# Kernel optimization log

Measured on AMD Instinct MI355X. Metric: run time of the kernel, lower is better.

Reference implementation:

```python
import jax, jax.numpy as jnp
import numpy as np

B, T, I, H, K = 32, 1024, 512, 512, 2


def _causal_conv1d(x_bit, w_hik, b_h):
    # x_bit: [B, I, T]; left-pad K-1 zeros (ConstantPad1d((K-1, 0)))
    xp = jnp.pad(x_bit, ((0, 0), (0, 0), (K - 1, 0)))
    y = jax.lax.conv_general_dilated(
        xp, w_hik, window_strides=(1,), padding='VALID',
        dimension_numbers=('NCH', 'OIH', 'NCH'))  # [B, H, T]
    return y + b_h[None, :, None]


def setup_inputs() -> dict:
    key = jax.random.key(0)
    k1, k2, k3 = jax.random.split(key, 3)
    bound = 1.0 / np.sqrt(I * K)  # torch Conv1d default init scale
    return {
        'inputs': jax.random.normal(k1, (B, T, I), dtype=jnp.float32),
        'init_state': jnp.zeros((B, H), dtype=jnp.float32),
        'Wz': jax.random.uniform(k2, (H, I, K), jnp.float32, -bound, bound),
        'bz': jnp.zeros((H,), dtype=jnp.float32),
        'Wf': jax.random.uniform(k3, (H, I, K), jnp.float32, -bound, bound),
        'bf': jnp.zeros((H,), dtype=jnp.float32),
    }


def reference(inputs, init_state, Wz, bz, Wf, bf):
    # init_state is accepted but unused in the original forward (mode='f').
    x = inputs.transpose(0, 2, 1)                      # [B, I, T]
    raw_f = _causal_conv1d(x, Wf, bf).transpose(0, 2, 1)  # [B, T, H]
    raw_z = _causal_conv1d(x, Wz, bz).transpose(0, 2, 1)  # [B, T, H]

    log_f = jax.nn.log_sigmoid(raw_f)
    log_one_minus_f = jax.nn.log_sigmoid(-raw_f)
    log_z = jax.nn.log_sigmoid(raw_z)

    # recurrent_gates[t] = sum_{s>t} log_f[s]  (suffix sum of log_f over time, excluding t=0 shift)
    rg = log_f[:, 1:, :]                               # [B, T-1, H]
    cs = jnp.cumsum(rg, axis=1)
    rg = rg - cs + cs[:, -1:, :]
    rg = jnp.concatenate([rg, jnp.zeros((inputs.shape[0], 1, rg.shape[2]), dtype=rg.dtype)], axis=1)  # [B, T, H]

    log_hidden = jax.lax.cumlogsumexp(log_z + log_one_minus_f + rg, axis=1)
    hidden = jnp.exp(log_hidden - rg)
    return hidden
```

## Files before the change

### kernel.cpp

```cpp
#include <hip/hip_runtime.h>
#include <hip/hip_bf16.h>
#include <cstddef>
#include <cstdint>

#define B_  32
#define T_  1024
#define I_  512
#define H_  512
#define M_  (B_ * T_)
#define TP_ 1025

typedef __bf16 bf16x8  __attribute__((ext_vector_type(8)));
typedef float  floatx4 __attribute__((ext_vector_type(4)));
typedef unsigned short ushort8v __attribute__((ext_vector_type(8)));
typedef unsigned long long u64;

__device__ __forceinline__ unsigned short f2bf(float f) {
    uint32_t u = __float_as_uint(f);
    return (unsigned short)((u + 0x7FFFu + ((u >> 16) & 1u)) >> 16);
}
__device__ __forceinline__ float sigm(float x) {
    return __builtin_amdgcn_rcpf(1.f + __expf(-x));
}

#define GLL(src, dst) __builtin_amdgcn_global_load_lds( \
    (const __attribute__((address_space(1))) void*)(src), \
    (__attribute__((address_space(3))) void*)(dst), 16, 0, 0)

#define NB_BUILD 8200
#define NB_PACK  512
#define NB_ZERO  256

__global__ __launch_bounds__(256) void prep(const float* __restrict__ x,
                                            const float* __restrict__ Wf,
                                            const float* __restrict__ Wz,
                                            unsigned short* __restrict__ Ab2,
                                            unsigned short* __restrict__ Wq,
                                            uint4* __restrict__ HpubZ,
                                            uint32_t* __restrict__ cnt) {
    if (blockIdx.x < NB_BUILD) {
        int g = blockIdx.x * 256 + threadIdx.x;
        int idx8 = g << 3;
        int row = idx8 >> 9;
        int col = idx8 & 511;
        int b    = (int)((unsigned)row / TP_);
        int trow = row - b * TP_;
        ushort8v o = {0, 0, 0, 0, 0, 0, 0, 0};
        if (trow > 0) {
            const float* src = &x[((size_t)b * T_ + (trow - 1)) * I_ + col];
            float4 v0 = *(const float4*)src;
            float4 v1 = *(const float4*)(src + 4);
            o[0] = f2bf(v0.x); o[1] = f2bf(v0.y); o[2] = f2bf(v0.z); o[3] = f2bf(v0.w);
            o[4] = f2bf(v1.x); o[5] = f2bf(v1.y); o[6] = f2bf(v1.z); o[7] = f2bf(v1.w);
        }
        *(ushort8v*)&Ab2[(size_t)idx8] = o;
    } else if (blockIdx.x < NB_BUILD + NB_PACK) {
        int cid = (blockIdx.x - NB_BUILD) * 256 + threadIdx.x;
        int lane = cid & 63;
        int c    = (cid >> 6) & 3;
        int wn   = (cid >> 8) & 1;
        int ksub = (cid >> 9) & 31;
        int ni   = (cid >> 14) & 3;
        int gate = (cid >> 16) & 1;
        int n_col = ni * 128 + wn * 64 + c * 16 + (lane & 15);
        const float* G = gate ? Wz : Wf;
        ushort8v o;
        #pragma unroll
        for (int j = 0; j < 8; ++j) {
            int k   = ksub * 32 + (lane >> 4) * 8 + j;
            int tap = k >> 9;
            int i   = k & 511;
            o[j] = f2bf(G[n_col * (I_ * 2) + i * 2 + tap]);
        }
        *(ushort8v*)&Wq[(size_t)cid * 8] = o;
    } else {
        int g = (blockIdx.x - NB_BUILD - NB_PACK) * 256 + threadIdx.x;
        HpubZ[g] = make_uint4(0, 0, 0, 0);
        if (g == 0) *cnt = 0;
    }
}

__global__ __launch_bounds__(256, 2) void mfma_gemm_scan(
        const unsigned short* __restrict__ Ab2,
        const unsigned short* __restrict__ Wq,
        const float* __restrict__ biasF,
        const float* __restrict__ biasZ,
        float* __restrict__ out,
        u64* __restrict__ Hpub,
        uint32_t* __restrict__ counter) {
    __shared__ unsigned short smem[24576];
    __shared__ uint32_t vid_s;

    const int tid = threadIdx.x;
    if (tid == 0) vid_s = atomicAdd(counter, 1u);
    __syncthreads();
    const int vid   = (int)vid_s;
    const int low3  = vid & 7;
    const int ni    = (vid >> 3) & 3;
    const int rem   = vid >> 5;
    const int pos   = rem >> 2;
    const int b     = ((rem & 3) << 3) | low3;
    const int chain = ni * 32 + b;
    const int h0    = ni * 128;
    const int browBase = b * TP_ + pos * 128;

    const int lane = tid & 63;
    const int wave = tid >> 6;
    const int wm   = wave >> 1, wn = wave & 1;
    const int lm   = lane & 15, quad = lane >> 4;

    const int c0 = wave * 128 + lane;
    const int c1 = c0 + 64;
    const int r0 = c0 >> 2, q0 = (c0 & 3) ^ ((r0 >> 2) & 3);
    const int r1 = c1 >> 2, q1 = (c1 & 3) ^ ((r1 >> 2) & 3);

    const unsigned short* pA0 = Ab2 + (size_t)(browBase + r0) * 512 + q0 * 8;
    const unsigned short* pA1 = Ab2 + (size_t)(browBase + r1) * 512 + q1 * 8;

    unsigned short* dA0 = smem + wave * 1024;
    unsigned short* dA1 = smem + wave * 1024 + 512;

    const unsigned short* wq = Wq + ni * 131072 + wn * 2048 + lane * 8;

    int offA[4];
    #pragma unroll
    for (int r = 0; r < 4; ++r) {
        int ml = wm * 64 + r * 16 + lm;
        offA[r] = (4 * ml + (quad ^ ((ml >> 2) & 3))) * 8;
    }

    floatx4 accF[4][4] = {};
    floatx4 accZ[4][4] = {};

    for (int kt2 = 0; kt2 < 16; ++kt2) {
        const int tap = kt2 >> 3;
        const int i0  = (kt2 & 7) * 64;
        #pragma unroll
        for (int s = 0; s < 2; ++s) {
            const int aoff = tap * 512 + i0 + s * 32;
            GLL(pA0 + aoff, dA0 + s * 4096);
            GLL(pA1 + aoff, dA1 + s * 4096);
        }
        __syncthreads();

        #pragma unroll
        for (int s = 0; s < 2; ++s) {
            const int ksub = kt2 * 2 + s;
            const unsigned short* wqk = wq + ksub * 4096;
            bf16x8 af[4], bF[4], bZ[4];
            #pragma unroll
            for (int c = 0; c < 4; ++c) {
                bF[c] = *(const bf16x8*)(wqk + c * 512);
                bZ[c] = *(const bf16x8*)(wqk + 524288 + c * 512);
            }
            #pragma unroll
            for (int r = 0; r < 4; ++r) af[r] = *(const bf16x8*)(smem + s * 4096 + offA[r]);
            #pragma unroll
            for (int r = 0; r < 4; ++r) {
                #pragma unroll
                for (int c = 0; c < 4; ++c) {
                    accF[r][c] = __builtin_amdgcn_mfma_f32_16x16x32_bf16(
                                    af[r], bF[c], accF[r][c], 0, 0, 0);
                    accZ[r][c] = __builtin_amdgcn_mfma_f32_16x16x32_bf16(
                                    af[r], bZ[c], accZ[r][c], 0, 0, 0);
                }
            }
        }
        __syncthreads();
    }

    float bfv[4], bzv[4];
    #pragma unroll
    for (int c = 0; c < 4; ++c) {
        int hc = h0 + wn * 64 + c * 16 + lm;
        bfv[c] = biasF[hc];
        bzv[c] = biasZ[hc];
    }

    float2* seg  = (float2*)smem;
    float*  hinL = (float*)&smem[16384];

    #pragma unroll
    for (int r = 0; r < 4; ++r) {
        const int sid = wm * 16 + r * 4 + quad;
        #pragma unroll
        for (int c = 0; c < 4; ++c) {
            float A = 1.f, C = 0.f;
            #pragma unroll
            for (int v = 0; v < 4; ++v) {
                float f = sigm(accF[r][c][v] + bfv[c]);
                float z = sigm(accZ[r][c][v] + bzv[c]);
                accF[r][c][v] = f;
                accZ[r][c][v] = z;
                A *= f;
                C = fmaf(f, C - z, z);
            }
            seg[sid * 128 + wn * 64 + c * 16 + lm] = make_float2(A, C);
        }
    }
    __syncthreads();

    float Hin = 0.f;
    if (tid < 128) {
        float At = 1.f, Ct = 0.f;
        #pragma unroll 8
        for (int s = 0; s < 32; ++s) {
            float2 sc = seg[s * 128 + tid];
            Ct = fmaf(sc.x, Ct, sc.y);
            At *= sc.x;
        }
        if (pos > 0) {
            u64* p = &Hpub[((size_t)(pos - 1) * 128 + chain) * 128 + tid];
            u64 v;
            while (((v = atomicAdd(p, 0ull)) >> 32) == 0ull)
                __builtin_amdgcn_s_sleep(2);
            Hin = __uint_as_float((uint32_t)v);
        }
        if (pos < 7) {
            float Hout = fmaf(At, Hin, Ct);
            u64 pv = 0x100000000ull | (u64)__float_as_uint(Hout);
            atomicExch(&Hpub[((size_t)pos * 128 + chain) * 128 + tid], pv);
        }
        float run = Hin;
        #pragma unroll 8
        for (int s = 0; s < 32; ++s) {
            hinL[s * 128 + tid] = run;
            float2 sc = seg[s * 128 + tid];
            run = fmaf(sc.x, run, sc.y);
        }
    }
    __syncthreads();

    const int rowBase = b * T_ + pos * 128;
    #pragma unroll
    for (int r = 0; r < 4; ++r) {
        const int sid = wm * 16 + r * 4 + quad;
        #pragma unroll
        for (int c = 0; c < 4; ++c) {
            const int hc = h0 + wn * 64 + c * 16 + lm;
            float hs = hinL[sid * 128 + (hc - h0)];
            #pragma unroll
            for (int v = 0; v < 4; ++v) {
                float f = accF[r][c][v];
                float z = accZ[r][c][v];
                hs = fmaf(f, hs - z, z);
                const size_t row = (size_t)(rowBase + wm * 64 + r * 16 + quad * 4 + v);
                out[row * H_ + hc] = hs;
            }
        }
    }
}

extern "C" void kernel_launch(void* const* d_in, const int* in_sizes, int n_in,
                              void* d_out, int out_size, void* d_ws, size_t ws_size,
                              hipStream_t stream) {
    const float* x  = (const float*)d_in[0];
    const float* Wz = (const float*)d_in[2];
    const float* bz = (const float*)d_in[3];
    const float* Wf = (const float*)d_in[4];
    const float* bf = (const float*)d_in[5];
    float* out = (float*)d_out;

    char* ws = (char*)d_ws;
    unsigned short* Ab2  = (unsigned short*)(ws);
    unsigned short* Wq   = (unsigned short*)(ws + (size_t)34 * 1024 * 1024);
    u64*            Hpub = (u64*)(ws + (size_t)36 * 1024 * 1024);
    uint32_t*       cnt  = (uint32_t*)(ws + (size_t)37 * 1024 * 1024);

    prep<<<NB_BUILD + NB_PACK + NB_ZERO, 256, 0, stream>>>(
        x, Wf, Wz, Ab2, Wq, (uint4*)Hpub, cnt);

    mfma_gemm_scan<<<1024, 256, 0, stream>>>(Ab2, Wq, bf, bz, out, Hpub, cnt);
}
```

Baseline: 202.1 us.

## Load A fragments directly from global with register double-buffering, drop LDS staging

Replaces the LDS staging of the A tile (global_load_lds plus two barriers per k-step) with direct per-lane global loads of A fragments into registers. Both A and B fragments are double-buffered in registers so the next k-substep's loads are issued before the current MFMAs. This removes the per-iteration __syncthreads and LDS traffic, at the cost of more VGPRs and redundant global A loads across the two wn waves, which now rely on cache.

```diff
diff --git a/kernel.cpp b/kernel.cpp
--- a/kernel.cpp
+++ b/kernel.cpp
@@ -22,10 +22,6 @@
 __device__ __forceinline__ float sigm(float x) {
     return __builtin_amdgcn_rcpf(1.f + __expf(-x));
 }
-
-#define GLL(src, dst) __builtin_amdgcn_global_load_lds( \
-    (const __attribute__((address_space(1))) void*)(src), \
-    (__attribute__((address_space(3))) void*)(dst), 16, 0, 0)
 
 #define NB_BUILD 8200
 #define NB_PACK  512
@@ -109,64 +105,53 @@
     const int wm   = wave >> 1, wn = wave & 1;
     const int lm   = lane & 15, quad = lane >> 4;
 
-    const int c0 = wave * 128 + lane;
-    const int c1 = c0 + 64;
-    const int r0 = c0 >> 2, q0 = (c0 & 3) ^ ((r0 >> 2) & 3);
-    const int r1 = c1 >> 2, q1 = (c1 & 3) ^ ((r1 >> 2) & 3);
-
-    const unsigned short* pA0 = Ab2 + (size_t)(browBase + r0) * 512 + q0 * 8;
-    const unsigned short* pA1 = Ab2 + (size_t)(browBase + r1) * 512 + q1 * 8;
-
-    unsigned short* dA0 = smem + wave * 1024;
-    unsigned short* dA1 = smem + wave * 1024 + 512;
-
-    const unsigned short* wq = Wq + ni * 131072 + wn * 2048 + lane * 8;
-
-    int offA[4];
-    #pragma unroll
-    for (int r = 0; r < 4; ++r) {
-        int ml = wm * 64 + r * 16 + lm;
-        offA[r] = (4 * ml + (quad ^ ((ml >> 2) & 3))) * 8;
-    }
+    const unsigned short* pA[4];
+    #pragma unroll
+    for (int r = 0; r < 4; ++r)
+        pA[r] = Ab2 + (size_t)(browBase + wm * 64 + r * 16 + lm) * 512 + quad * 8;
+
+    const unsigned short* bqF = Wq + ni * 131072 + wn * 2048 + lane * 8;
+    const unsigned short* bqZ = bqF + 524288;
+
+    bf16x8 af[2][4], bF[2][4], bZ[2][4];
+
+#define LOADS(KSUB, BUF) do {                                            \
+        const int _ao = (((KSUB) >> 4) * 512) + (((KSUB) & 15) * 32);    \
+        _Pragma("unroll")                                                \
+        for (int _r = 0; _r < 4; ++_r)                                   \
+            af[BUF][_r] = *(const bf16x8*)(pA[_r] + _ao);                \
+        const unsigned short* _pF = bqF + (KSUB) * 4096;                 \
+        const unsigned short* _pZ = bqZ + (KSUB) * 4096;                 \
+        _Pragma("unroll")                                                \
+        for (int _c = 0; _c < 4; ++_c) {                                 \
+            bF[BUF][_c] = *(const bf16x8*)(_pF + _c * 512);              \
+            bZ[BUF][_c] = *(const bf16x8*)(_pZ + _c * 512);              \
+        }                                                                \
+    } while (0)
+
+#define MFMAS(BUF) do {                                                  \
+        _Pragma("unroll")                                                \
+        for (int _r = 0; _r < 4; ++_r) {                                 \
+            _Pragma("unroll")                                            \
+            for (int _c = 0; _c < 4; ++_c) {                             \
+                accF[_r][_c] = __builtin_amdgcn_mfma_f32_16x16x32_bf16(  \
+                    af[BUF][_r], bF[BUF][_c], accF[_r][_c], 0, 0, 0);    \
+                accZ[_r][_c] = __builtin_amdgcn_mfma_f32_16x16x32_bf16(  \
+                    af[BUF][_r], bZ[BUF][_c], accZ[_r][_c], 0, 0, 0);    \
+            }                                                            \
+        }                                                                \
+    } while (0)
 
     floatx4 accF[4][4] = {};
     floatx4 accZ[4][4] = {};
 
-    for (int kt2 = 0; kt2 < 16; ++kt2) {
-        const int tap = kt2 >> 3;
-        const int i0  = (kt2 & 7) * 64;
-        #pragma unroll
-        for (int s = 0; s < 2; ++s) {
-            const int aoff = tap * 512 + i0 + s * 32;
-            GLL(pA0 + aoff, dA0 + s * 4096);
-            GLL(pA1 + aoff, dA1 + s * 4096);
-        }
-        __syncthreads();
-
-        #pragma unroll
-        for (int s = 0; s < 2; ++s) {
-            const int ksub = kt2 * 2 + s;
-            const unsigned short* wqk = wq + ksub * 4096;
-            bf16x8 af[4], bF[4], bZ[4];
-            #pragma unroll
-            for (int c = 0; c < 4; ++c) {
-                bF[c] = *(const bf16x8*)(wqk + c * 512);
-                bZ[c] = *(const bf16x8*)(wqk + 524288 + c * 512);
-            }
-            #pragma unroll
-            for (int r = 0; r < 4; ++r) af[r] = *(const bf16x8*)(smem + s * 4096 + offA[r]);
-            #pragma unroll
-            for (int r = 0; r < 4; ++r) {
-                #pragma unroll
-                for (int c = 0; c < 4; ++c) {
-                    accF[r][c] = __builtin_amdgcn_mfma_f32_16x16x32_bf16(
-                                    af[r], bF[c], accF[r][c], 0, 0, 0);
-                    accZ[r][c] = __builtin_amdgcn_mfma_f32_16x16x32_bf16(
-                                    af[r], bZ[c], accZ[r][c], 0, 0, 0);
-                }
-            }
-        }
-        __syncthreads();
+    LOADS(0, 0);
+    for (int kk2 = 0; kk2 < 16; ++kk2) {
+        const int ksub = kk2 * 2;
+        LOADS(ksub + 1, 1);
+        MFMAS(0);
+        if (kk2 < 15) LOADS(ksub + 2, 0);
+        MFMAS(1);
     }
 
     float bfv[4], bzv[4];
```

Result: slower. 229.8 us (+13.7%).
